# Kernel tuning notes

Measured on AMD Instinct MI355X. Metric: run time of the kernel, lower is better.

## Reference

```python
import jax, jax.numpy as jnp
import numpy as np

D_MODEL = 512
HEADS = 8

def setup_inputs() -> dict:
    key = jax.random.key(0)
    ks = jax.random.split(key, 11)
    B, S, D = 2, 4096, D_MODEL
    s = 1.0 / np.sqrt(D)
    inp = {
        'q': jax.random.normal(ks[0], (B, S, D), jnp.float32),
        'k': jax.random.normal(ks[1], (B, S, D), jnp.float32),
        'v': jax.random.normal(ks[2], (B, S, D), jnp.float32),
        'Wq': jax.random.normal(ks[3], (D, D), jnp.float32) * s,
        'bq': jnp.zeros((D,), jnp.float32),
        'Wk': jax.random.normal(ks[4], (D, D), jnp.float32) * s,
        'bk': jnp.zeros((D,), jnp.float32),
        'Wv': jax.random.normal(ks[5], (D, D), jnp.float32) * s,
        'bv': jnp.zeros((D,), jnp.float32),
        'Wo': jax.random.normal(ks[6], (D, D), jnp.float32) * s,
        'bo': jnp.zeros((D,), jnp.float32),
    }
    return inp

def _split_heads(x, h):
    B, S, D = x.shape
    return x.reshape(B, S, h, D // h).transpose(0, 2, 1, 3)  # [B,H,S,Dh]

def reference(q, k, v, Wq, bq, Wk, bk, Wv, bv, Wo, bo):
    # torch Linear: y = x @ W.T + b
    qh = _split_heads(q @ Wq.T + bq, HEADS)
    kh = _split_heads(k @ Wk.T + bk, HEADS)
    vh = _split_heads(v @ Wv.T + bv, HEADS)
    d_tensor = qh.shape[-1]
    scale = 1.0 / jnp.sqrt(jnp.asarray(d_tensor, qh.dtype))
    score = jnp.einsum('bhqd,bhkd->bhqk', qh, kh) * scale  # [B,H,S,S]
    attn = jax.nn.softmax(score, axis=-1)
    out = jnp.einsum('bhqk,bhkd->bhqd', attn, vh)
    B, H, S, Dh = out.shape
    out = out.transpose(0, 2, 1, 3).reshape(B, S, H * Dh)
    return out @ Wo.T + bo
```

## Files before the change

### kernel.cpp

```cpp
#include <hip/hip_runtime.h>

typedef short bf16x8 __attribute__((ext_vector_type(8)));
typedef float f32x2 __attribute__((ext_vector_type(2)));
typedef float f32x4 __attribute__((ext_vector_type(4)));
typedef float f32x16 __attribute__((ext_vector_type(16)));
typedef unsigned short ushort_t;
typedef unsigned short us8 __attribute__((ext_vector_type(8)));
typedef unsigned short us4 __attribute__((ext_vector_type(4)));
typedef unsigned int u32x4 __attribute__((ext_vector_type(4)));
typedef unsigned int uint2v __attribute__((ext_vector_type(2)));

#define MFMA16(a, b, c) __builtin_amdgcn_mfma_f32_16x16x32_bf16((a), (b), (c), 0, 0, 0)
#define MFMA32(a, b, c) __builtin_amdgcn_mfma_f32_32x32x16_bf16((a), (b), (c), 0, 0, 0)

template <int N> struct ic { static constexpr int value = N; };

static __device__ __forceinline__ ushort_t f2bf(float f) {
    unsigned int u = __builtin_bit_cast(unsigned int, f);
    u += 0x7FFFu + ((u >> 16) & 1u);
    return (ushort_t)(u >> 16);
}

static __device__ __forceinline__ unsigned cvtpk(float lo, float hi) {
    unsigned r;
    asm("v_cvt_pk_bf16_f32 %0, %1, %2" : "=v"(r) : "v"(lo), "v"(hi));
    return r;
}

static __device__ __forceinline__ void gload16(const void* g, void* l) {
    __builtin_amdgcn_global_load_lds(
        (const __attribute__((address_space(1))) unsigned int*)g,
        (__attribute__((address_space(3))) unsigned int*)l,
        16, 0, 0);
}

__global__ __launch_bounds__(256) void cvt_w(const float* __restrict__ W0,
                                             const float* __restrict__ W1,
                                             const float* __restrict__ W2,
                                             const float* __restrict__ W3,
                                             ushort_t* __restrict__ dst) {
    const float* src = (blockIdx.y == 0) ? W0 : (blockIdx.y == 1) ? W1
                     : (blockIdx.y == 2) ? W2 : W3;
    const int i = (blockIdx.x * 256 + threadIdx.x) * 8;
    float4 f0 = *(const float4*)(src + i);
    float4 f1 = *(const float4*)(src + i + 4);
    unsigned tw[4] = {cvtpk(f0.x, f0.y), cvtpk(f0.z, f0.w),
                      cvtpk(f1.x, f1.y), cvtpk(f1.z, f1.w)};
    *(u32x4*)(dst + (size_t)blockIdx.y * 262144 + i) = *(u32x4*)tw;
}

__global__ __launch_bounds__(256) void gemm_qkv(const float* __restrict__ qi,
                                                const float* __restrict__ ki,
                                                const float* __restrict__ vi,
                                                const ushort_t* __restrict__ Wball,
                                                const float* __restrict__ bq,
                                                const float* __restrict__ bk,
                                                const float* __restrict__ bv,
                                                ushort_t* __restrict__ Qh,
                                                ushort_t* __restrict__ Kh,
                                                ushort_t* __restrict__ Vt,
                                                float Cs) {
    constexpr int K = 512;
    __shared__ ushort_t As[64][72];
    __shared__ ushort_t Bs[64][72];

    const int which = blockIdx.y;
    const float*    Ap   = (which == 0) ? qi : (which == 1) ? ki : vi;
    const ushort_t* Wb   = Wball + (size_t)which * 262144;
    const float*    bias = (which == 0) ? bq : (which == 1) ? bk : bv;
    ushort_t*       outp = (which == 0) ? Qh : (which == 1) ? Kh : Vt;

    int bid = blockIdx.x;
    bid = (bid & 7) * 128 + (bid >> 3);
    const int bm = bid >> 3;
    const int bn = bid & 7;
    const int m0 = bm * 64, n0 = bn * 64;
    const int t    = threadIdx.x;
    const int lane = t & 63;
    const int wv   = t >> 6;
    const int wm   = wv >> 1, wn = wv & 1;
    const int lrow = t >> 2;
    const int lcol = (t & 3) * 16;

    const int l15 = lane & 15;
    const int l16 = lane >> 4;

    f32x4 acc[2][2] = {};

    const float*    apf = Ap + (size_t)(m0 + lrow) * K + lcol;
    const ushort_t* bpb = Wb + (size_t)(n0 + lrow) * K + lcol;

    us8 br0, br1;
    f32x4 af[4];

    af[0] = *(const f32x4*)apf;       af[1] = *(const f32x4*)(apf + 4);
    af[2] = *(const f32x4*)(apf + 8); af[3] = *(const f32x4*)(apf + 12);
    br0 = *(const us8*)bpb; br1 = *(const us8*)(bpb + 8);

#pragma unroll 1
    for (int kt = 0; kt < K / 64; ++kt) {
        __syncthreads();
        {
            unsigned tw[8];
#pragma unroll
            for (int i = 0; i < 4; ++i) {
                tw[2 * i]     = cvtpk(af[i][0], af[i][1]);
                tw[2 * i + 1] = cvtpk(af[i][2], af[i][3]);
            }
            *(u32x4*)&As[lrow][lcol]     = *(u32x4*)tw;
            *(u32x4*)&As[lrow][lcol + 8] = *(u32x4*)(tw + 4);
        }
        *(us8*)&Bs[lrow][lcol]     = br0;
        *(us8*)&Bs[lrow][lcol + 8] = br1;
        __syncthreads();

        if (kt < K / 64 - 1) {
            const int off = (kt + 1) * 64;
            const float* s = apf + off;
            af[0] = *(const f32x4*)s;       af[1] = *(const f32x4*)(s + 4);
            af[2] = *(const f32x4*)(s + 8); af[3] = *(const f32x4*)(s + 12);
            br0 = *(const us8*)(bpb + off); br1 = *(const us8*)(bpb + off + 8);
        }

#pragma unroll
        for (int kk = 0; kk < 2; ++kk) {
            bf16x8 a0 = *(const bf16x8*)&As[wm * 32 + l15][kk * 32 + l16 * 8];
            bf16x8 a1 = *(const bf16x8*)&As[wm * 32 + 16 + l15][kk * 32 + l16 * 8];
            bf16x8 b0 = *(const bf16x8*)&Bs[wn * 32 + l15][kk * 32 + l16 * 8];
            bf16x8 b1 = *(const bf16x8*)&Bs[wn * 32 + 16 + l15][kk * 32 + l16 * 8];
            acc[0][0] = MFMA16(a0, b0, acc[0][0]);
            acc[0][1] = MFMA16(a0, b1, acc[0][1]);
            acc[1][0] = MFMA16(a1, b0, acc[1][0]);
            acc[1][1] = MFMA16(a1, b1, acc[1][1]);
        }
    }

#pragma unroll
    for (int i = 0; i < 2; ++i)
#pragma unroll
        for (int j = 0; j < 2; ++j) {
            const int n  = n0 + wn * 32 + j * 16 + l15;
            const float bv_ = bias[n];
            const int h = n >> 6, d = n & 63;
            if (which == 2) {
                const int mbase = m0 + wm * 32 + i * 16 + l16 * 4;
                const int b = mbase >> 12, key = mbase & 4095;
                const int keyr = key & 63;
                const int ks = keyr >> 4, hc = (keyr >> 3) & 1, e0 = keyr & 7;
                const int db = d >> 5, dr = d & 31;
                ushort_t tmp[4];
#pragma unroll
                for (int v = 0; v < 4; ++v) tmp[v] = f2bf(acc[i][j][v] + bv_);
                *(us4*)(outp + (size_t)(b * 8 + h) * 262144 +
                        (size_t)(key >> 6) * 4096 +
                        db * 2048 + ks * 512 + (hc * 32 + dr) * 8 + e0) = *(us4*)tmp;
            } else if (which == 1) {
                const int jd = d >> 4, hc = (d >> 3) & 1, e = d & 7;
#pragma unroll
                for (int v = 0; v < 4; ++v) {
                    const int m = m0 + wm * 32 + i * 16 + l16 * 4 + v;
                    const int b = m >> 12, s = m & 4095;
                    const int r = s & 63, kb2 = r >> 5, kr = r & 31;
                    outp[(size_t)(b * 8 + h) * 262144 + (size_t)(s >> 6) * 4096 +
                         kb2 * 2048 + jd * 512 + (hc * 32 + kr) * 8 + e] =
                        f2bf(acc[i][j][v] + bv_);
                }
            } else {
#pragma unroll
                for (int v = 0; v < 4; ++v) {
                    const int m = m0 + wm * 32 + i * 16 + l16 * 4 + v;
                    const int b = m >> 12, s = m & 4095;
                    outp[(((size_t)(b * 8 + h)) * 4096 + s) * 64 + d] =
                        f2bf((acc[i][j][v] + bv_) * Cs);
                }
            }
        }
}

__global__ __launch_bounds__(256) void gemm_out(const ushort_t* __restrict__ Ap,
                                                const ushort_t* __restrict__ Wb,
                                                const float* __restrict__ bias,
                                                float* __restrict__ outp) {
    constexpr int K = 512;
    __shared__ ushort_t As[64][72];
    __shared__ ushort_t Bs[64][72];

    int bid = blockIdx.x;
    bid = (bid & 7) * 128 + (bid >> 3);
    const int bm = bid >> 3;
    const int bn = bid & 7;
    const int m0 = bm * 64, n0 = bn * 64;
    const int t    = threadIdx.x;
    const int lane = t & 63;
    const int wv   = t >> 6;
    const int wm   = wv >> 1, wn = wv & 1;
    const int lrow = t >> 2;
    const int lcol = (t & 3) * 16;

    const int l15 = lane & 15;
    const int l16 = lane >> 4;

    f32x4 acc[2][2] = {};

    const ushort_t* apb = Ap + (size_t)(m0 + lrow) * K + lcol;
    const ushort_t* bpb = Wb + (size_t)(n0 + lrow) * K + lcol;

    us8 ar0, ar1, br0, br1;
    ar0 = *(const us8*)apb; ar1 = *(const us8*)(apb + 8);
    br0 = *(const us8*)bpb; br1 = *(const us8*)(bpb + 8);

#pragma unroll 1
    for (int kt = 0; kt < K / 64; ++kt) {
        __syncthreads();
        *(us8*)&As[lrow][lcol]     = ar0;
        *(us8*)&As[lrow][lcol + 8] = ar1;
        *(us8*)&Bs[lrow][lcol]     = br0;
        *(us8*)&Bs[lrow][lcol + 8] = br1;
        __syncthreads();

        if (kt < K / 64 - 1) {
            const int off = (kt + 1) * 64;
            ar0 = *(const us8*)(apb + off); ar1 = *(const us8*)(apb + off + 8);
            br0 = *(const us8*)(bpb + off); br1 = *(const us8*)(bpb + off + 8);
        }

#pragma unroll
        for (int kk = 0; kk < 2; ++kk) {
            bf16x8 a0 = *(const bf16x8*)&As[wm * 32 + l15][kk * 32 + l16 * 8];
            bf16x8 a1 = *(const bf16x8*)&As[wm * 32 + 16 + l15][kk * 32 + l16 * 8];
            bf16x8 b0 = *(const bf16x8*)&Bs[wn * 32 + l15][kk * 32 + l16 * 8];
            bf16x8 b1 = *(const bf16x8*)&Bs[wn * 32 + 16 + l15][kk * 32 + l16 * 8];
            acc[0][0] = MFMA16(a0, b0, acc[0][0]);
            acc[0][1] = MFMA16(a0, b1, acc[0][1]);
            acc[1][0] = MFMA16(a1, b0, acc[1][0]);
            acc[1][1] = MFMA16(a1, b1, acc[1][1]);
        }
    }

#pragma unroll
    for (int i = 0; i < 2; ++i)
#pragma unroll
        for (int j = 0; j < 2; ++j) {
            const int n  = n0 + wn * 32 + j * 16 + l15;
            const float bv_ = bias[n];
#pragma unroll
            for (int v = 0; v < 4; ++v) {
                const int m = m0 + wm * 32 + i * 16 + l16 * 4 + v;
                outp[(size_t)m * 512 + n] = acc[i][j][v] + bv_;
            }
        }
}

__global__ __launch_bounds__(256) void attn_fwd(const ushort_t* __restrict__ Qh,
                                                const ushort_t* __restrict__ Kg,
                                                const ushort_t* __restrict__ Vg,
                                                ushort_t* __restrict__ Out) {
    constexpr int S  = 4096;
    constexpr int NT = 64;
    __shared__ __attribute__((aligned(16))) char LDS[32768];

    const int qt = blockIdx.x;
    const int bh = blockIdx.y;
    const int b  = bh >> 3, h = bh & 7;

    const int t    = threadIdx.x;
    const int lane = t & 63;
    const int wv   = t >> 6;
    const int l31  = lane & 31;
    const int hl   = lane >> 5;

    const int qw = qt * 128 + wv * 32;

    bf16x8 qf[4];
    {
        const ushort_t* qp = Qh + ((size_t)bh * S + qw + l31) * 64 + hl * 8;
#pragma unroll
        for (int ds = 0; ds < 4; ++ds) qf[ds] = *(const bf16x8*)(qp + ds * 16);
    }

    const f32x16 fzero = {};
    f32x16 accO[2] = {};
    float ll = 0.f;

    const char* lbase = LDS + lane * 16;
    const int wvb = wv * 1024;
    const ushort_t* kg = Kg + (size_t)bh * 262144 + wv * 512 + lane * 8;
    const ushort_t* vg = Vg + (size_t)bh * 262144 + wv * 512 + lane * 8;

    auto issue = [&](int kt, auto curc) {
        constexpr int CUR = decltype(curc)::value;
        const ushort_t* kg_ = kg + (size_t)kt * 4096;
        const ushort_t* vg_ = vg + (size_t)kt * 4096;
        gload16(kg_,        LDS + CUR * 8192 + wvb);
        gload16(kg_ + 2048, LDS + CUR * 8192 + 4096 + wvb);
        gload16(vg_,        LDS + 16384 + CUR * 8192 + wvb);
        gload16(vg_ + 2048, LDS + 16384 + CUR * 8192 + 4096 + wvb);
    };

    auto tile = [&](int kt, auto curc) {
        constexpr int CUR = decltype(curc)::value;

        f32x16 sc0, sc1;
        __builtin_amdgcn_s_setprio(1);
        {
            bf16x8 kf = *(const bf16x8*)(lbase + CUR * 8192);
            sc0 = MFMA32(kf, qf[0], fzero);
        }
#pragma unroll
        for (int ds = 1; ds < 4; ++ds) {
            bf16x8 kf = *(const bf16x8*)(lbase + CUR * 8192 + ds * 1024);
            sc0 = MFMA32(kf, qf[ds], sc0);
        }
        {
            bf16x8 kf = *(const bf16x8*)(lbase + CUR * 8192 + 4096);
            sc1 = MFMA32(kf, qf[0], fzero);
        }
#pragma unroll
        for (int ds = 1; ds < 4; ++ds) {
            bf16x8 kf = *(const bf16x8*)(lbase + CUR * 8192 + 4096 + ds * 1024);
            sc1 = MFMA32(kf, qf[ds], sc1);
        }
        __builtin_amdgcn_s_setprio(0);

#pragma unroll
        for (int i = 0; i < 16; ++i) {
            sc0[i] = __builtin_amdgcn_exp2f(sc0[i]);
            sc1[i] = __builtin_amdgcn_exp2f(sc1[i]);
        }

        {
#define PAIR(v, i) __builtin_shufflevector((v), (v), 2 * (i), 2 * (i) + 1)
            f32x2 pa = (PAIR(sc0, 0) + PAIR(sc0, 1)) + (PAIR(sc0, 2) + PAIR(sc0, 3));
            f32x2 pbt = (PAIR(sc0, 4) + PAIR(sc0, 5)) + (PAIR(sc0, 6) + PAIR(sc0, 7));
            f32x2 pc = (PAIR(sc1, 0) + PAIR(sc1, 1)) + (PAIR(sc1, 2) + PAIR(sc1, 3));
            f32x2 pd = (PAIR(sc1, 4) + PAIR(sc1, 5)) + (PAIR(sc1, 6) + PAIR(sc1, 7));
            f32x2 s2 = (pa + pbt) + (pc + pd);
            ll += s2.x + s2.y;
#undef PAIR
        }

        bf16x8 pb[4];
#pragma unroll
        for (int ks = 0; ks < 4; ++ks) {
            const int R0 = (ks & 1) * 8;
            float e0, e1, e2, e3, e4, e5, e6, e7;
            if (ks < 2) {
                e0 = sc0[R0+0]; e1 = sc0[R0+1]; e2 = sc0[R0+2]; e3 = sc0[R0+3];
                e4 = sc0[R0+4]; e5 = sc0[R0+5]; e6 = sc0[R0+6]; e7 = sc0[R0+7];
            } else {
                e0 = sc1[R0+0]; e1 = sc1[R0+1]; e2 = sc1[R0+2]; e3 = sc1[R0+3];
                e4 = sc1[R0+4]; e5 = sc1[R0+5]; e6 = sc1[R0+6]; e7 = sc1[R0+7];
            }
            unsigned w0 = cvtpk(e0, e1);
            unsigned w1 = cvtpk(e2, e3);
            unsigned w2 = cvtpk(e4, e5);
            unsigned w3 = cvtpk(e6, e7);
            uint2v s02 = __builtin_amdgcn_permlane32_swap(w0, w2, false, false);
            uint2v s13 = __builtin_amdgcn_permlane32_swap(w1, w3, false, false);
            u32x4 w = {s02.x, s13.x, s02.y, s13.y};
            pb[ks] = __builtin_bit_cast(bf16x8, w);
        }

        __builtin_amdgcn_s_setprio(1);
#pragma unroll
        for (int ks = 0; ks < 4; ++ks) {
            {
                bf16x8 vf = *(const bf16x8*)(lbase + 16384 + CUR * 8192 + ks * 1024);
                accO[0] = MFMA32(vf, pb[ks], accO[0]);
            }
            {
                bf16x8 vf = *(const bf16x8*)(lbase + 16384 + CUR * 8192 + 4096 + ks * 1024);
                accO[1] = MFMA32(vf, pb[ks], accO[1]);
            }
        }
        __builtin_amdgcn_s_setprio(0);

        __syncthreads();
        if (kt + 2 < NT) issue(kt + 2, curc);
    };

    issue(0, ic<0>{});
    issue(1, ic<1>{});
    __syncthreads();

#pragma unroll 1
    for (int kt2 = 0; kt2 < NT; kt2 += 2) {
        tile(kt2,     ic<0>{});
        tile(kt2 + 1, ic<1>{});
    }

    const float lt  = ll + __shfl_xor(ll, 32);
    const float inv = 1.0f / lt;
    ushort_t* orow = Out + ((size_t)b * S + qw + l31) * 512 + h * 64;
#pragma unroll
    for (int db = 0; db < 2; ++db)
#pragma unroll
        for (int q4 = 0; q4 < 4; ++q4) {
            unsigned w0 = cvtpk(accO[db][q4 * 4 + 0] * inv, accO[db][q4 * 4 + 1] * inv);
            unsigned w1 = cvtpk(accO[db][q4 * 4 + 2] * inv, accO[db][q4 * 4 + 3] * inv);
            unsigned tmp[2] = {w0, w1};
            *(us4*)(orow + db * 32 + q4 * 8 + hl * 4) = *(const us4*)tmp;
        }
}

extern "C" void kernel_launch(void* const* d_in, const int* in_sizes, int n_in,
                              void* d_out, int out_size, void* d_ws, size_t ws_size,
                              hipStream_t stream) {
    const float* q  = (const float*)d_in[0];
    const float* k  = (const float*)d_in[1];
    const float* v  = (const float*)d_in[2];
    const float* Wq = (const float*)d_in[3];
    const float* bq = (const float*)d_in[4];
    const float* bk = (const float*)d_in[6];
    const float* bv = (const float*)d_in[8];
    const float* bo = (const float*)d_in[10];

    char* w = (char*)d_ws;
    const size_t SZ = (size_t)2 * 8 * 4096 * 64 * 2;

    ushort_t* Qh  = (ushort_t*)(w);
    ushort_t* Kh  = (ushort_t*)(w + SZ);
    ushort_t* Vtr = (ushort_t*)(w + 2 * SZ);
    ushort_t* AO  = (ushort_t*)(w + 3 * SZ);
    ushort_t* Wb  = (ushort_t*)(w + 4 * SZ);

    cvt_w<<<dim3(128, 4), 256, 0, stream>>>(Wq, (const float*)d_in[5],
                                            (const float*)d_in[7], (const float*)d_in[9], Wb);

    const float Cs = 0.125f * 1.44269504f;
    gemm_qkv<<<dim3(1024, 3), 256, 0, stream>>>(q, k, v, Wb, bq, bk, bv, Qh, Kh, Vtr, Cs);

    attn_fwd<<<dim3(32, 16), 256, 0, stream>>>(Qh, Kh, Vtr, AO);

    gemm_out<<<1024, 256, 0, stream>>>(AO, Wb + 3 * 262144, bo, (float*)d_out);
}
```

Before: 140.4 us.

## Enlarge GEMM tiles, use direct global-to-LDS loads, MFMA row sums, XCD-aware attention grid

New measurement: 147.7 us. +5.2%, slower.

```diff
diff --git a/kernel.cpp b/kernel.cpp
--- a/kernel.cpp
+++ b/kernel.cpp
@@ -1,7 +1,6 @@
 #include <hip/hip_runtime.h>
 
 typedef short bf16x8 __attribute__((ext_vector_type(8)));
-typedef float f32x2 __attribute__((ext_vector_type(2)));
 typedef float f32x4 __attribute__((ext_vector_type(4)));
 typedef float f32x16 __attribute__((ext_vector_type(16)));
 typedef unsigned short ushort_t;
@@ -60,9 +59,8 @@
                                                 ushort_t* __restrict__ Kh,
                                                 ushort_t* __restrict__ Vt,
                                                 float Cs) {
-    constexpr int K = 512;
-    __shared__ ushort_t As[64][72];
-    __shared__ ushort_t Bs[64][72];
+    __shared__ __attribute__((aligned(16))) ushort_t As[128][32];
+    __shared__ __attribute__((aligned(16))) ushort_t Bs[128][32];
 
     const int which = blockIdx.y;
     const float*    Ap   = (which == 0) ? qi : (which == 1) ? ki : vi;
@@ -70,80 +68,75 @@
     const float*    bias = (which == 0) ? bq : (which == 1) ? bk : bv;
     ushort_t*       outp = (which == 0) ? Qh : (which == 1) ? Kh : Vt;
 
-    int bid = blockIdx.x;
-    bid = (bid & 7) * 128 + (bid >> 3);
-    const int bm = bid >> 3;
-    const int bn = bid & 7;
-    const int m0 = bm * 64, n0 = bn * 64;
+    const int bid = blockIdx.x;
+    const int rid = (bid & 7) * 32 + (bid >> 3);
+    const int bm  = rid >> 2, bn = rid & 3;
+    const int m0  = bm * 128, n0 = bn * 128;
+
     const int t    = threadIdx.x;
     const int lane = t & 63;
     const int wv   = t >> 6;
     const int wm   = wv >> 1, wn = wv & 1;
-    const int lrow = t >> 2;
-    const int lcol = (t & 3) * 16;
-
-    const int l15 = lane & 15;
-    const int l16 = lane >> 4;
-
-    f32x4 acc[2][2] = {};
-
-    const float*    apf = Ap + (size_t)(m0 + lrow) * K + lcol;
-    const ushort_t* bpb = Wb + (size_t)(n0 + lrow) * K + lcol;
-
-    us8 br0, br1;
-    f32x4 af[4];
-
-    af[0] = *(const f32x4*)apf;       af[1] = *(const f32x4*)(apf + 4);
-    af[2] = *(const f32x4*)(apf + 8); af[3] = *(const f32x4*)(apf + 12);
-    br0 = *(const us8*)bpb; br1 = *(const us8*)(bpb + 8);
+    const int l15  = lane & 15, l16 = lane >> 4;
+    const int srow = t >> 2;
+    const int scol = (t & 3) * 8;
+
+    f32x4 acc[4][4] = {};
+
+    const float*    a0p = Ap + (size_t)(m0 + srow) * 512 + scol;
+    const float*    a1p = a0p + (size_t)64 * 512;
+    const ushort_t* b0p = Wb + (size_t)(n0 + srow) * 512 + scol;
+    const ushort_t* b1p = b0p + (size_t)64 * 512;
+
+    f32x4 ar[4];
+    ar[0] = *(const f32x4*)a0p; ar[1] = *(const f32x4*)(a0p + 4);
+    ar[2] = *(const f32x4*)a1p; ar[3] = *(const f32x4*)(a1p + 4);
 
 #pragma unroll 1
-    for (int kt = 0; kt < K / 64; ++kt) {
+    for (int kt = 0; kt < 16; ++kt) {
         __syncthreads();
         {
-            unsigned tw[8];
-#pragma unroll
-            for (int i = 0; i < 4; ++i) {
-                tw[2 * i]     = cvtpk(af[i][0], af[i][1]);
-                tw[2 * i + 1] = cvtpk(af[i][2], af[i][3]);
-            }
-            *(u32x4*)&As[lrow][lcol]     = *(u32x4*)tw;
-            *(u32x4*)&As[lrow][lcol + 8] = *(u32x4*)(tw + 4);
-        }
-        *(us8*)&Bs[lrow][lcol]     = br0;
-        *(us8*)&Bs[lrow][lcol + 8] = br1;
+            unsigned t0[4] = {cvtpk(ar[0][0], ar[0][1]), cvtpk(ar[0][2], ar[0][3]),
+                              cvtpk(ar[1][0], ar[1][1]), cvtpk(ar[1][2], ar[1][3])};
+            *(u32x4*)&As[srow][scol] = *(u32x4*)t0;
+            unsigned t1[4] = {cvtpk(ar[2][0], ar[2][1]), cvtpk(ar[2][2], ar[2][3]),
+                              cvtpk(ar[3][0], ar[3][1]), cvtpk(ar[3][2], ar[3][3])};
+            *(u32x4*)&As[64 + srow][scol] = *(u32x4*)t1;
+        }
+        gload16(b0p + kt * 32, (char*)Bs + wv * 1024);
+        gload16(b1p + kt * 32, (char*)Bs + 4096 + wv * 1024);
         __syncthreads();
 
-        if (kt < K / 64 - 1) {
-            const int off = (kt + 1) * 64;
-            const float* s = apf + off;
-            af[0] = *(const f32x4*)s;       af[1] = *(const f32x4*)(s + 4);
-            af[2] = *(const f32x4*)(s + 8); af[3] = *(const f32x4*)(s + 12);
-            br0 = *(const us8*)(bpb + off); br1 = *(const us8*)(bpb + off + 8);
-        }
-
-#pragma unroll
-        for (int kk = 0; kk < 2; ++kk) {
-            bf16x8 a0 = *(const bf16x8*)&As[wm * 32 + l15][kk * 32 + l16 * 8];
-            bf16x8 a1 = *(const bf16x8*)&As[wm * 32 + 16 + l15][kk * 32 + l16 * 8];
-            bf16x8 b0 = *(const bf16x8*)&Bs[wn * 32 + l15][kk * 32 + l16 * 8];
-            bf16x8 b1 = *(const bf16x8*)&Bs[wn * 32 + 16 + l15][kk * 32 + l16 * 8];
-            acc[0][0] = MFMA16(a0, b0, acc[0][0]);
-            acc[0][1] = MFMA16(a0, b1, acc[0][1]);
-            acc[1][0] = MFMA16(a1, b0, acc[1][0]);
-            acc[1][1] = MFMA16(a1, b1, acc[1][1]);
-        }
+        if (kt < 15) {
+            const float* an0 = a0p + (kt + 1) * 32;
+            const float* an1 = a1p + (kt + 1) * 32;
+            ar[0] = *(const f32x4*)an0; ar[1] = *(const f32x4*)(an0 + 4);
+            ar[2] = *(const f32x4*)an1; ar[3] = *(const f32x4*)(an1 + 4);
+        }
+
+        bf16x8 af[4], bf[4];
+#pragma unroll
+        for (int i = 0; i < 4; ++i)
+            af[i] = *(const bf16x8*)&As[wm * 64 + i * 16 + l15][l16 * 8];
+#pragma unroll
+        for (int j = 0; j < 4; ++j)
+            bf[j] = *(const bf16x8*)&Bs[wn * 64 + j * 16 + l15][l16 * 8];
+#pragma unroll
+        for (int i = 0; i < 4; ++i)
+#pragma unroll
+            for (int j = 0; j < 4; ++j)
+                acc[i][j] = MFMA16(af[i], bf[j], acc[i][j]);
     }
 
 #pragma unroll
-    for (int i = 0; i < 2; ++i)
-#pragma unroll
-        for (int j = 0; j < 2; ++j) {
-            const int n  = n0 + wn * 32 + j * 16 + l15;
+    for (int i = 0; i < 4; ++i)
+#pragma unroll
+        for (int j = 0; j < 4; ++j) {
+            const int n  = n0 + wn * 64 + j * 16 + l15;
             const float bv_ = bias[n];
             const int h = n >> 6, d = n & 63;
             if (which == 2) {
-                const int mbase = m0 + wm * 32 + i * 16 + l16 * 4;
+                const int mbase = m0 + wm * 64 + i * 16 + l16 * 4;
                 const int b = mbase >> 12, key = mbase & 4095;
                 const int keyr = key & 63;
                 const int ks = keyr >> 4, hc = (keyr >> 3) & 1, e0 = keyr & 7;
@@ -158,7 +151,7 @@
                 const int jd = d >> 4, hc = (d >> 3) & 1, e = d & 7;
 #pragma unroll
                 for (int v = 0; v < 4; ++v) {
-                    const int m = m0 + wm * 32 + i * 16 + l16 * 4 + v;
+                    const int m = m0 + wm * 64 + i * 16 + l16 * 4 + v;
                     const int b = m >> 12, s = m & 4095;
                     const int r = s & 63, kb2 = r >> 5, kr = r & 31;
                     outp[(size_t)(b * 8 + h) * 262144 + (size_t)(s >> 6) * 4096 +
@@ -168,7 +161,7 @@
             } else {
 #pragma unroll
                 for (int v = 0; v < 4; ++v) {
-                    const int m = m0 + wm * 32 + i * 16 + l16 * 4 + v;
+                    const int m = m0 + wm * 64 + i * 16 + l16 * 4 + v;
                     const int b = m >> 12, s = m & 4095;
                     outp[(((size_t)(b * 8 + h)) * 4096 + s) * 64 + d] =
                         f2bf((acc[i][j][v] + bv_) * Cs);
@@ -181,71 +174,59 @@
                                                 const ushort_t* __restrict__ Wb,
                                                 const float* __restrict__ bias,
                                                 float* __restrict__ outp) {
-    constexpr int K = 512;
-    __shared__ ushort_t As[64][72];
-    __shared__ ushort_t Bs[64][72];
-
-    int bid = blockIdx.x;
-    bid = (bid & 7) * 128 + (bid >> 3);
-    const int bm = bid >> 3;
-    const int bn = bid & 7;
-    const int m0 = bm * 64, n0 = bn * 64;
+    __shared__ __attribute__((aligned(16))) ushort_t As[128][32];
+    __shared__ __attribute__((aligned(16))) ushort_t Bs[64][32];
+
+    const int bid = blockIdx.x;
+    const int rid = (bid & 7) * 64 + (bid >> 3);
+    const int bm  = rid >> 3, bn = rid & 7;
+    const int m0  = bm * 128, n0 = bn * 64;
+
     const int t    = threadIdx.x;
     const int lane = t & 63;
     const int wv   = t >> 6;
     const int wm   = wv >> 1, wn = wv & 1;
-    const int lrow = t >> 2;
-    const int lcol = (t & 3) * 16;
-
-    const int l15 = lane & 15;
-    const int l16 = lane >> 4;
-
-    f32x4 acc[2][2] = {};
-
-    const ushort_t* apb = Ap + (size_t)(m0 + lrow) * K + lcol;
-    const ushort_t* bpb = Wb + (size_t)(n0 + lrow) * K + lcol;
-
-    us8 ar0, ar1, br0, br1;
-    ar0 = *(const us8*)apb; ar1 = *(const us8*)(apb + 8);
-    br0 = *(const us8*)bpb; br1 = *(const us8*)(bpb + 8);
+    const int l15  = lane & 15, l16 = lane >> 4;
+    const int srow = t >> 2;
+    const int scol = (t & 3) * 8;
+
+    f32x4 acc[4][2] = {};
+
+    const ushort_t* a0p = Ap + (size_t)(m0 + srow) * 512 + scol;
+    const ushort_t* a1p = a0p + (size_t)64 * 512;
+    const ushort_t* b0p = Wb + (size_t)(n0 + srow) * 512 + scol;
 
 #pragma unroll 1
-    for (int kt = 0; kt < K / 64; ++kt) {
+    for (int kt = 0; kt < 16; ++kt) {
         __syncthreads();
-        *(us8*)&As[lrow][lcol]     = ar0;
-        *(us8*)&As[lrow][lcol + 8] = ar1;
-        *(us8*)&Bs[lrow][lcol]     = br0;
-        *(us8*)&Bs[lrow][lcol + 8] = br1;
+        gload16(a0p + kt * 32, (char*)As + wv * 1024);
+        gload16(a1p + kt * 32, (char*)As + 4096 + wv * 1024);
+        gload16(b0p + kt * 32, (char*)Bs + wv * 1024);
         __syncthreads();
 
-        if (kt < K / 64 - 1) {
-            const int off = (kt + 1) * 64;
-            ar0 = *(const us8*)(apb + off); ar1 = *(const us8*)(apb + off + 8);
-            br0 = *(const us8*)(bpb + off); br1 = *(const us8*)(bpb + off + 8);
-        }
-
-#pragma unroll
-        for (int kk = 0; kk < 2; ++kk) {
-            bf16x8 a0 = *(const bf16x8*)&As[wm * 32 + l15][kk * 32 + l16 * 8];
-            bf16x8 a1 = *(const bf16x8*)&As[wm * 32 + 16 + l15][kk * 32 + l16 * 8];
-            bf16x8 b0 = *(const bf16x8*)&Bs[wn * 32 + l15][kk * 32 + l16 * 8];
-            bf16x8 b1 = *(const bf16x8*)&Bs[wn * 32 + 16 + l15][kk * 32 + l16 * 8];
-            acc[0][0] = MFMA16(a0, b0, acc[0][0]);
-            acc[0][1] = MFMA16(a0, b1, acc[0][1]);
-            acc[1][0] = MFMA16(a1, b0, acc[1][0]);
-            acc[1][1] = MFMA16(a1, b1, acc[1][1]);
-        }
+        bf16x8 af[4], bf[2];
+#pragma unroll
+        for (int i = 0; i < 4; ++i)
+            af[i] = *(const bf16x8*)&As[wm * 64 + i * 16 + l15][l16 * 8];
+#pragma unroll
+        for (int j = 0; j < 2; ++j)
+            bf[j] = *(const bf16x8*)&Bs[wn * 32 + j * 16 + l15][l16 * 8];
+#pragma unroll
+        for (int i = 0; i < 4; ++i)
+#pragma unroll
+            for (int j = 0; j < 2; ++j)
+                acc[i][j] = MFMA16(af[i], bf[j], acc[i][j]);
     }
 
 #pragma unroll
-    for (int i = 0; i < 2; ++i)
+    for (int i = 0; i < 4; ++i)
 #pragma unroll
         for (int j = 0; j < 2; ++j) {
             const int n  = n0 + wn * 32 + j * 16 + l15;
             const float bv_ = bias[n];
 #pragma unroll
             for (int v = 0; v < 4; ++v) {
-                const int m = m0 + wm * 32 + i * 16 + l16 * 4 + v;
+                const int m = m0 + wm * 64 + i * 16 + l16 * 4 + v;
                 outp[(size_t)m * 512 + n] = acc[i][j][v] + bv_;
             }
         }
@@ -259,9 +240,12 @@
     constexpr int NT = 64;
     __shared__ __attribute__((aligned(16))) char LDS[32768];
 
-    const int qt = blockIdx.x;
-    const int bh = blockIdx.y;
-    const int b  = bh >> 3, h = bh & 7;
+    const int id   = blockIdx.x;
+    const int xcd  = id & 7;
+    const int slot = id >> 3;
+    const int qt   = slot & 31;
+    const int bh   = xcd * 2 + (slot >> 5);
+    const int b    = bh >> 3, h = bh & 7;
 
     const int t    = threadIdx.x;
     const int lane = t & 63;
@@ -278,9 +262,13 @@
         for (int ds = 0; ds < 4; ++ds) qf[ds] = *(const bf16x8*)(qp + ds * 16);
     }
 
+    bf16x8 ones;
+#pragma unroll
+    for (int j = 0; j < 8; ++j) ones[j] = (short)0x3F80;
+
     const f32x16 fzero = {};
     f32x16 accO[2] = {};
-    float ll = 0.f;
+    f32x16 lacc = {};
 
     const char* lbase = LDS + lane * 16;
     const int wvb = wv * 1024;
@@ -326,17 +314,6 @@
         for (int i = 0; i < 16; ++i) {
             sc0[i] = __builtin_amdgcn_exp2f(sc0[i]);
             sc1[i] = __builtin_amdgcn_exp2f(sc1[i]);
-        }
-
-        {
-#define PAIR(v, i) __builtin_shufflevector((v), (v), 2 * (i), 2 * (i) + 1)
-            f32x2 pa = (PAIR(sc0, 0) + PAIR(sc0, 1)) + (PAIR(sc0, 2) + PAIR(sc0, 3));
-            f32x2 pbt = (PAIR(sc0, 4) + PAIR(sc0, 5)) + (PAIR(sc0, 6) + PAIR(sc0, 7));
-            f32x2 pc = (PAIR(sc1, 0) + PAIR(sc1, 1)) + (PAIR(sc1, 2) + PAIR(sc1, 3));
-            f32x2 pd = (PAIR(sc1, 4) + PAIR(sc1, 5)) + (PAIR(sc1, 6) + PAIR(sc1, 7));
-            f32x2 s2 = (pa + pbt) + (pc + pd);
-            ll += s2.x + s2.y;
-#undef PAIR
         }
 
         bf16x8 pb[4];
@@ -372,6 +349,7 @@
                 bf16x8 vf = *(const bf16x8*)(lbase + 16384 + CUR * 8192 + 4096 + ks * 1024);
                 accO[1] = MFMA32(vf, pb[ks], accO[1]);
             }
+            lacc = MFMA32(ones, pb[ks], lacc);
         }
         __builtin_amdgcn_s_setprio(0);
 
@@ -389,7 +367,7 @@
         tile(kt2 + 1, ic<1>{});
     }
 
-    const float lt  = ll + __shfl_xor(ll, 32);
+    const float lt  = lacc[0];
     const float inv = 1.0f / lt;
     ushort_t* orow = Out + ((size_t)b * S + qw + l31) * 512 + h * 64;
 #pragma unroll
@@ -428,9 +406,9 @@
                                             (const float*)d_in[7], (const float*)d_in[9], Wb);
 
     const float Cs = 0.125f * 1.44269504f;
-    gemm_qkv<<<dim3(1024, 3), 256, 0, stream>>>(q, k, v, Wb, bq, bk, bv, Qh, Kh, Vtr, Cs);
-
-    attn_fwd<<<dim3(32, 16), 256, 0, stream>>>(Qh, Kh, Vtr, AO);
-
-    gemm_out<<<1024, 256, 0, stream>>>(AO, Wb + 3 * 262144, bo, (float*)d_out);
-}
+    gemm_qkv<<<dim3(256, 3), 256, 0, stream>>>(q, k, v, Wb, bq, bk, bv, Qh, Kh, Vtr, Cs);
+
+    attn_fwd<<<512, 256, 0, stream>>>(Qh, Kh, Vtr, AO);
+
+    gemm_out<<<512, 256, 0, stream>>>(AO, Wb + 3 * 262144, bo, (float*)d_out);
+}
```
